# Performance work log

Measured on AMD Instinct MI355X. Metric: run time of the kernel, lower is better.

## Reference

```python
import jax, jax.numpy as jnp
import numpy as np

A = 5            # num_anchors
NC = 20          # num_classes
IGNORE_THRESH = 0.6
COORD_SCALE = 1.0
NOOBJ_SCALE = 1.0
OBJ_SCALE = 5.0
CLASS_SCALE = 1.0
ANCHORS_NP = np.array([[0.052, 0.066], [0.14, 0.11], [0.24, 0.30], [0.45, 0.42], [0.77, 0.72]], dtype=np.float32)


def setup_inputs() -> dict:
    key = jax.random.key(0)
    k1, k2, k3, k4, k5 = jax.random.split(key, 5)
    B, F, O = 32, 38, 50
    C = A * (5 + NC)
    outputs = jax.random.normal(k1, (B, C, F, F), jnp.float32)
    # targets: (cx, cy, w, h, cls) normalized; padded rows are all-zero
    cxy = jax.random.uniform(k2, (B, O, 2), minval=0.15, maxval=0.85)
    wh = jax.random.uniform(k3, (B, O, 2), minval=0.05, maxval=0.20)
    cls = jax.random.randint(k4, (B, O), 0, NC).astype(jnp.float32)
    targets = jnp.concatenate([cxy, wh, cls[..., None]], axis=-1)
    nobj = jax.random.randint(k5, (B,), 10, O + 1)
    valid = (jnp.arange(O)[None, :] < nobj[:, None]).astype(jnp.float32)
    targets = targets * valid[..., None]
    return {"outputs": outputs, "targets": targets, "anchors": jnp.asarray(ANCHORS_NP)}


def _pairwise_iou_xywh(a, b):
    # a: (..., N, 4), b: (..., M, 4) center-format -> IoU (..., N, M)
    a = a[..., :, None, :]
    b = b[..., None, :, :]
    tl = jnp.maximum(a[..., :2] - a[..., 2:] * 0.5, b[..., :2] - b[..., 2:] * 0.5)
    br = jnp.minimum(a[..., :2] + a[..., 2:] * 0.5, b[..., :2] + b[..., 2:] * 0.5)
    wh = jnp.clip(br - tl, 0.0)
    inter = wh[..., 0] * wh[..., 1]
    area_a = a[..., 2] * a[..., 3]
    area_b = b[..., 2] * b[..., 3]
    return inter / (area_a + area_b - inter + 1e-12)


def _forward(outputs, targets, anchors):
    B, C, F, _ = outputs.shape
    S = F * F
    O = targets.shape[1]
    valid = targets.sum(axis=2) > 0                    # (B, O)
    gt = targets[..., :4] * F                          # grid-unit cxywh
    gt_cls = targets[..., 4]

    out5 = outputs.reshape(B, A, 5 + NC, F, F)
    jj = jnp.arange(F, dtype=outputs.dtype)            # x (last axis)
    ii = jnp.arange(F, dtype=outputs.dtype)[:, None]   # y
    aw = (anchors[:, 0] * F)[None, :, None, None]
    ah = (anchors[:, 1] * F)[None, :, None, None]
    px = jax.nn.sigmoid(out5[:, :, 0]) + jj
    py = jax.nn.sigmoid(out5[:, :, 1]) + ii
    pw = jnp.exp(out5[:, :, 2]) * aw
    ph = jnp.exp(out5[:, :, 3]) * ah
    pred_boxes = jnp.stack([px, py, pw, ph], -1).transpose(0, 2, 3, 1, 4).reshape(B, S * A, 4)

    # anchor prior boxes at cell centers: (S, A, 4)
    ax = jnp.broadcast_to(jj + 0.5, (F, F))
    ay = jnp.broadcast_to(ii + 0.5, (F, F))
    aa = jnp.stack([
        jnp.broadcast_to(ax[:, :, None], (F, F, A)),
        jnp.broadcast_to(ay[:, :, None], (F, F, A)),
        jnp.broadcast_to((anchors[:, 0] * F)[None, None, :], (F, F, A)),
        jnp.broadcast_to((anchors[:, 1] * F)[None, None, :], (F, F, A)),
    ], -1).reshape(S, A, 4)

    ious = _pairwise_iou_xywh(pred_boxes, gt)          # (B, S*A, O)
    ious = jnp.where(valid[:, None, :], ious, 0.0)     # padded objs excluded (IoU >= 0)
    max_iou = ious.reshape(B, S, A, O).max(axis=-1)    # (B, S, A)

    n_pos = jnp.any(max_iou > IGNORE_THRESH, axis=(1, 2))
    iou_mask = jnp.full((B, S, A), NOOBJ_SCALE, outputs.dtype)
    iou_mask = jnp.where(n_pos[:, None, None] & (max_iou >= IGNORE_THRESH), 0.0, iou_mask)

    overlaps = _pairwise_iou_xywh(aa.reshape(1, S * A, 4), gt).reshape(B, S, A, O)

    # responsible cell: floor of top-left corner (faithful to source), anchor = argmax prior overlap
    x1y1 = gt[..., :2] - gt[..., 2:] * 0.5
    cxcy = jnp.floor(x1y1).astype(jnp.int32)
    cell = jnp.clip(cxcy[..., 1] * F + cxcy[..., 0], 0, S - 1)             # (B, O)
    ovT = overlaps.transpose(0, 3, 1, 2)                                   # (B, O, S, A)
    ov_cell = jnp.take_along_axis(ovT, cell[:, :, None, None], axis=2)[:, :, 0, :]
    anchor_idx = jnp.argmax(ov_cell, axis=-1)                              # (B, O)
    resp = aa[cell, anchor_idx]                                            # (B, O, 4)
    deltas = jnp.stack([gt[..., 0] - resp[..., 0], gt[..., 1] - resp[..., 1],
                        gt[..., 2] / resp[..., 2], gt[..., 3] / resp[..., 3]], -1)
    mi = jnp.take_along_axis(jnp.take_along_axis(max_iou, cell[:, :, None], axis=1),
                             anchor_idx[:, :, None], axis=2)[..., 0]       # (B, O)

    b_rep = jnp.broadcast_to(jnp.arange(B)[:, None], (B, O))
    cell_s = jnp.where(valid, cell, S)  # OOB index for padded objs -> dropped
    zt = jnp.zeros((B, S, A), outputs.dtype)
    box_target = jnp.zeros((B, S, A, 4), outputs.dtype).at[b_rep, cell_s, anchor_idx].set(deltas, mode='drop')
    box_mask = zt.at[b_rep, cell_s, anchor_idx].set(1.0, mode='drop')
    class_target = zt.at[b_rep, cell_s, anchor_idx].set(gt_cls, mode='drop')
    class_mask = zt.at[b_rep, cell_s, anchor_idx].set(1.0, mode='drop')
    iou_target = zt.at[b_rep, cell_s, anchor_idx].set(mi, mode='drop')
    iou_mask = iou_mask.at[b_rep, cell_s, anchor_idx].set(OBJ_SCALE, mode='drop')

    # prediction side, layout (B, (i*F+j)*A + a, 5+NC) matching target layout
    outs = out5.transpose(0, 3, 4, 1, 2).reshape(B, S * A, 5 + NC)
    pd = jnp.concatenate([jax.nn.sigmoid(outs[..., :2]), jnp.exp(outs[..., 2:4])], -1)
    conf = jax.nn.sigmoid(outs[..., 4])
    probs = jax.nn.softmax(outs[..., 5:], axis=-1)

    bm = box_mask.reshape(B, S * A, 1)
    im = iou_mask.reshape(B, S * A)
    box_loss = jnp.sum((pd * bm - box_target.reshape(B, S * A, 4) * bm) ** 2)
    iou_loss = jnp.sum((conf * im - iou_target.reshape(B, S * A) * im) ** 2)
    # faithful quirk of the source: cross-entropy applied to softmax *outputs* as logits
    ls = jax.nn.log_softmax(probs, axis=-1)
    ct = class_target.reshape(B, S * A).astype(jnp.int32)
    ce = -jnp.take_along_axis(ls, ct[..., None], axis=-1)[..., 0]
    class_loss = jnp.sum(ce * class_mask.reshape(B, S * A))
    return (COORD_SCALE * box_loss + iou_loss + CLASS_SCALE * class_loss) / B


def reference(outputs, targets, anchors):
    return _forward(outputs, targets, anchors)
```

## Files before the change

kernel.cpp:

```cpp
#include <hip/hip_runtime.h>
#include <math.h>

#define A_N 5
#define NC 20
#define FD 38
#define SD (FD*FD)
#define BD 32
#define OD 50
#define SA (SD*A_N)
#define GX ((SA + 255) / 256)
#define NBLK (BD * GX)
#define IGN_T 0.6f
#define OBJ_S 5.0f

__device__ __forceinline__ float sigm(float x) { return 1.0f / (1.0f + __expf(-x)); }

__global__ __launch_bounds__(256) void k_main(
    const float* __restrict__ outputs, const float* __restrict__ targets,
    const float* __restrict__ anchors,
    float* __restrict__ pbase, float* __restrict__ pcorr, int* __restrict__ pflag,
    float* __restrict__ out)
{
    __shared__ float  s_traw[OD * 5];
    __shared__ float4 g_box[OD];
    __shared__ float  g_den[OD];
    __shared__ float  s_anc[2 * A_N];
    __shared__ int    s_cnt, s_any;
    __shared__ float  wb[4], wc[4];

    const int b = blockIdx.y;
    const int tid = threadIdx.x;
    if (tid == 0) { s_cnt = 0; s_any = 0; }
    if (tid < OD * 5)  s_traw[tid] = targets[b * (OD * 5) + tid];
    if (tid < 2 * A_N) s_anc[tid]  = anchors[tid];
    if (blockIdx.x == 0 && b == 0 && tid == 0) *out = 0.0f;

    const int idx = blockIdx.x * 256 + tid;
    const bool act = (idx < SA);
    const int a = idx / SD, s = idx - a * SD;
    const int i = s / FD, j = s - i * FD;
    const float* ob = outputs + ((size_t)b * (A_N * 25) + a * 25) * SD + s;
    float q0 = 0, q1 = 0, q2 = 0, q3 = 0, q4 = 0;
    if (act) { q0 = ob[0]; q1 = ob[SD]; q2 = ob[2*SD]; q3 = ob[3*SD]; q4 = ob[4*SD]; }
    __syncthreads();

    if (tid < OD) {
        float tx = s_traw[tid*5], ty = s_traw[tid*5+1], tw = s_traw[tid*5+2];
        float th = s_traw[tid*5+3], tc = s_traw[tid*5+4];
        if (tx + ty + tw + th + tc > 0.0f) {
            float gx = tx * FD, gy = ty * FD, gw = tw * FD, gh = th * FD;
            int k = atomicAdd(&s_cnt, 1);
            g_box[k] = make_float4(gx - gw*0.5f, gy - gh*0.5f, gx + gw*0.5f, gy + gh*0.5f);
            g_den[k] = gw * gh + 1e-12f;
        }
    }
    __syncthreads();
    const int cnt = s_cnt;

    float base = 0.0f, corr = 0.0f;
    bool hot = false;
    if (act) {
        float aw = s_anc[2*a] * FD, ah = s_anc[2*a+1] * FD;
        float px = sigm(q0) + (float)j;
        float py = sigm(q1) + (float)i;
        float pw = __expf(q2) * aw;
        float ph = __expf(q3) * ah;
        float tlx = px - pw*0.5f, tly = py - ph*0.5f;
        float brx = px + pw*0.5f, bry = py + ph*0.5f;
        float ar = pw * ph;
        float bn = 0.0f, bd = 1.0f;
        for (int o = 0; o < cnt; ++o) {
            float4 bx = g_box[o];
            float w = fmaxf(fminf(brx, bx.z) - fmaxf(tlx, bx.x), 0.0f);
            float h = fmaxf(fminf(bry, bx.w) - fmaxf(tly, bx.y), 0.0f);
            float in = w * h, de = ar + g_den[o] - in;
            if (in * bd > bn * de) { bn = in; bd = de; }
        }
        float t = IGN_T * bd;
        hot = (bn > t);
        float conf = sigm(q4);
        float c2 = conf * conf;
        if (bn >= t) corr += c2;
        else         base += c2;
    }

    unsigned long long bal = __ballot(hot);
    if ((tid & 63) == 0 && bal) atomicOr(&s_any, 1);

    #pragma unroll
    for (int off = 32; off > 0; off >>= 1) {
        base += __shfl_down(base, off);
        corr += __shfl_down(corr, off);
    }
    int lane = tid & 63, w = tid >> 6;
    if (lane == 0) { wb[w] = base; wc[w] = corr; }
    __syncthreads();
    if (tid == 0) {
        int gid = b * GX + blockIdx.x;
        pbase[gid] = wb[0] + wb[1] + wb[2] + wb[3];
        pcorr[gid] = wc[0] + wc[1] + wc[2] + wc[3];
        pflag[gid] = s_any;
    }
}

__global__ __launch_bounds__(64) void k_rf(
    const float* __restrict__ outputs, const float* __restrict__ targets,
    const float* __restrict__ anchors,
    const float* __restrict__ pbase, const float* __restrict__ pcorr,
    const int* __restrict__ pflag, float* __restrict__ out)
{
    __shared__ float  s_traw[OD * 5];
    __shared__ float4 g_box[OD];
    __shared__ float  g_den[OD];
    __shared__ float  s_anc[2 * A_N];
    __shared__ int    s_key[OD];
    __shared__ int    s_cnt;

    const int b = blockIdx.x;
    const int lane = threadIdx.x;
    if (lane == 0) s_cnt = 0;
    for (int t = lane; t < OD * 5; t += 64) s_traw[t] = targets[b * (OD * 5) + t];
    if (lane < 2 * A_N) s_anc[lane] = anchors[lane];
    __syncthreads();

    float gx = 0, gy = 0, gw = 0, gh = 0;
    int ct = 0, key = -1;
    if (lane < OD) {
        float tx = s_traw[lane*5], ty = s_traw[lane*5+1], tw = s_traw[lane*5+2];
        float th = s_traw[lane*5+3], tc = s_traw[lane*5+4];
        if (tx + ty + tw + th + tc > 0.0f) {
            gx = tx * FD; gy = ty * FD; gw = tw * FD; gh = th * FD;
            float gtlx = gx - gw*0.5f, gtly = gy - gh*0.5f;
            float gbrx = gx + gw*0.5f, gbry = gy + gh*0.5f;
            int k = atomicAdd(&s_cnt, 1);
            g_box[k] = make_float4(gtlx, gtly, gbrx, gbry);
            g_den[k] = gw * gh + 1e-12f;
            int cx = (int)floorf(gtlx), cy = (int)floorf(gtly);
            int cell = min(max(cy * FD + cx, 0), SD - 1);
            int ci = cell / FD, cj = cell - ci * FD;
            float acx = (float)cj + 0.5f, acy = (float)ci + 0.5f;
            float areaB = gw * gh;
            float best = -1.0f; int bi = 0;
            for (int a = 0; a < A_N; ++a) {
                float aw = s_anc[2*a] * FD, ah = s_anc[2*a+1] * FD;
                float w = fmaxf(fminf(acx + aw*0.5f, gbrx) - fmaxf(acx - aw*0.5f, gtlx), 0.0f);
                float h = fmaxf(fminf(acy + ah*0.5f, gbry) - fmaxf(acy - ah*0.5f, gtly), 0.0f);
                float inter = w * h;
                float iou = inter / (aw*ah + areaB - inter + 1e-12f);
                if (iou > best) { best = iou; bi = a; }
            }
            key = bi * SD + cell;
            ct = (int)tc;
        }
    }
    if (lane < OD) s_key[lane] = key;
    __syncthreads();
    const int cnt = s_cnt;

    float rbase = 0.0f, rcorr = 0.0f;
    if (lane < OD && key >= 0) {
        int win = -1;
        #pragma unroll 10
        for (int o = 0; o < OD; ++o) win = (s_key[o] == key) ? o : win;
        if (win == lane) {
            int a = key / SD, cell = key - a * SD;
            int ci = cell / FD, cj = cell - ci * FD;
            const float* ob = outputs + ((size_t)b * (A_N * 25) + a * 25) * SD + cell;
            float o0 = ob[0], o1 = ob[SD], o2 = ob[2*SD], o3 = ob[3*SD], o4 = ob[4*SD];
            float aw = s_anc[2*a] * FD, ah = s_anc[2*a+1] * FD;
            float px = sigm(o0) + (float)cj;
            float py = sigm(o1) + (float)ci;
            float ew = __expf(o2), eh = __expf(o3);
            float pw = ew * aw, ph = eh * ah;
            float tlx = px - pw*0.5f, tly = py - ph*0.5f;
            float brx = px + pw*0.5f, bry = py + ph*0.5f;
            float ar = pw * ph;
            float bn = 0.0f, bd = 1.0f;
            for (int o = 0; o < cnt; ++o) {
                float4 bx = g_box[o];
                float w = fmaxf(fminf(brx, bx.z) - fmaxf(tlx, bx.x), 0.0f);
                float h = fmaxf(fminf(bry, bx.w) - fmaxf(tly, bx.y), 0.0f);
                float in = w * h, de = ar + g_den[o] - in;
                if (in * bd > bn * de) { bn = in; bd = de; }
            }
            float mi = bn / bd;
            float conf = sigm(o4);
            float d = conf - mi;
            rbase += OBJ_S * OBJ_S * d * d;
            float c2 = conf * conf;
            if (bn >= IGN_T * bd) rcorr -= c2;
            else                  rbase -= c2;
            float dx = gx - ((float)cj + 0.5f);
            float dy = gy - ((float)ci + 0.5f);
            float e0 = sigm(o0) - dx;
            float e1 = sigm(o1) - dy;
            float e2 = ew - gw / aw;
            float e3 = eh - gh / ah;
            rbase += e0*e0 + e1*e1 + e2*e2 + e3*e3;
            float x[NC];
            float xmax = -INFINITY;
            #pragma unroll
            for (int k = 0; k < NC; ++k) { x[k] = ob[(5 + k) * SD]; xmax = fmaxf(xmax, x[k]); }
            float esum = 0.0f;
            #pragma unroll
            for (int k = 0; k < NC; ++k) { x[k] = __expf(x[k] - xmax); esum += x[k]; }
            float inv = 1.0f / esum;
            float pmax = 0.0f, pct = 0.0f;
            #pragma unroll
            for (int k = 0; k < NC; ++k) {
                float p = x[k] * inv; x[k] = p;
                pmax = fmaxf(pmax, p);
                pct = (k == ct) ? p : pct;
            }
            float e2s = 0.0f;
            #pragma unroll
            for (int k = 0; k < NC; ++k) e2s += __expf(x[k] - pmax);
            rbase += -(pct - (pmax + __logf(e2s)));
        }
    }

    float pb = 0.0f, pc = 0.0f;
    int fl = 0;
    if (lane < GX) {
        pb = pbase[b * GX + lane];
        pc = pcorr[b * GX + lane];
        fl = pflag[b * GX + lane];
    }
    int np = (__ballot(fl != 0) != 0ull) ? 1 : 0;
    float sb = rbase + pb, sc = rcorr + pc;
    #pragma unroll
    for (int off = 32; off > 0; off >>= 1) {
        sb += __shfl_down(sb, off);
        sc += __shfl_down(sc, off);
    }
    if (lane == 0) {
        float total = sb + (np ? 0.0f : sc);
        atomicAdd(out, total * (1.0f / (float)BD));
    }
}

extern "C" void kernel_launch(void* const* d_in, const int* in_sizes, int n_in,
                              void* d_out, int out_size, void* d_ws, size_t ws_size,
                              hipStream_t stream) {
    (void)in_sizes; (void)n_in; (void)out_size; (void)ws_size;
    const float* outputs = (const float*)d_in[0];
    const float* targets = (const float*)d_in[1];
    const float* anchors = (const float*)d_in[2];
    float* out = (float*)d_out;

    float* pbase = (float*)d_ws;
    float* pcorr = pbase + NBLK;
    int*   pflag = (int*)(pcorr + NBLK);

    k_main<<<dim3(GX, BD), 256, 0, stream>>>(outputs, targets, anchors,
                                             pbase, pcorr, pflag, out);
    k_rf<<<dim3(BD), 64, 0, stream>>>(outputs, targets, anchors,
                                      pbase, pcorr, pflag, out);
}
```

Before: 83.84 us.

## Fold responsible-anchor work into main kernel and process two predictions per thread

The per-batch responsible-anchor computation moves from the second kernel into an extra block of the main grid, so it runs alongside the IoU scan. Each main-kernel thread now handles two anchor-cells, sharing every ground-truth box load across both IoU computations and halving the number of blocks. The second kernel becomes a tiny single-block reduction that writes the output directly, which removes the atomic add and the zero-initialisation. In exchange, parallelism per batch drops to 15 blocks plus one serial-ish block per batch, and the extra block adds latency to the critical path.

```diff
diff --git a/kernel.cpp b/kernel.cpp
--- a/kernel.cpp
+++ b/kernel.cpp
@@ -8,8 +8,10 @@
 #define BD 32
 #define OD 50
 #define SA (SD*A_N)
-#define GX ((SA + 255) / 256)
-#define NBLK (BD * GX)
+#define HALF (SA/2)
+#define GXP 15
+#define SLOTB 16
+#define NSLOT (BD * SLOTB)
 #define IGN_T 0.6f
 #define OBJ_S 5.0f
 
@@ -18,35 +20,152 @@
 __global__ __launch_bounds__(256) void k_main(
     const float* __restrict__ outputs, const float* __restrict__ targets,
     const float* __restrict__ anchors,
-    float* __restrict__ pbase, float* __restrict__ pcorr, int* __restrict__ pflag,
-    float* __restrict__ out)
+    float* __restrict__ pbase, float* __restrict__ pcorr, int* __restrict__ pflag)
 {
-    __shared__ float  s_traw[OD * 5];
     __shared__ float4 g_box[OD];
     __shared__ float  g_den[OD];
     __shared__ float  s_anc[2 * A_N];
     __shared__ int    s_cnt, s_any;
+    __shared__ int    s_key[OD];
     __shared__ float  wb[4], wc[4];
 
     const int b = blockIdx.y;
     const int tid = threadIdx.x;
     if (tid == 0) { s_cnt = 0; s_any = 0; }
-    if (tid < OD * 5)  s_traw[tid] = targets[b * (OD * 5) + tid];
-    if (tid < 2 * A_N) s_anc[tid]  = anchors[tid];
-    if (blockIdx.x == 0 && b == 0 && tid == 0) *out = 0.0f;
-
-    const int idx = blockIdx.x * 256 + tid;
-    const bool act = (idx < SA);
-    const int a = idx / SD, s = idx - a * SD;
-    const int i = s / FD, j = s - i * FD;
-    const float* ob = outputs + ((size_t)b * (A_N * 25) + a * 25) * SD + s;
-    float q0 = 0, q1 = 0, q2 = 0, q3 = 0, q4 = 0;
-    if (act) { q0 = ob[0]; q1 = ob[SD]; q2 = ob[2*SD]; q3 = ob[3*SD]; q4 = ob[4*SD]; }
-    __syncthreads();
-
+    if (tid < 2 * A_N) s_anc[tid] = anchors[tid];
+
+    if (blockIdx.x == GXP) {
+        __syncthreads();
+        float gx = 0, gy = 0, gw = 0, gh = 0;
+        int ct = 0, key = -1;
+        if (tid < OD) {
+            const float* t = targets + (b * OD + tid) * 5;
+            float tx = t[0], ty = t[1], tw = t[2], th = t[3], tc = t[4];
+            if (tx + ty + tw + th + tc > 0.0f) {
+                gx = tx * FD; gy = ty * FD; gw = tw * FD; gh = th * FD;
+                float gtlx = gx - gw*0.5f, gtly = gy - gh*0.5f;
+                float gbrx = gx + gw*0.5f, gbry = gy + gh*0.5f;
+                int k = atomicAdd(&s_cnt, 1);
+                g_box[k] = make_float4(gtlx, gtly, gbrx, gbry);
+                g_den[k] = gw * gh + 1e-12f;
+                int cx = (int)floorf(gtlx), cy = (int)floorf(gtly);
+                int cell = min(max(cy * FD + cx, 0), SD - 1);
+                int ci = cell / FD, cj = cell - ci * FD;
+                float acx = (float)cj + 0.5f, acy = (float)ci + 0.5f;
+                float areaB = gw * gh;
+                float best = -1.0f; int bi = 0;
+                for (int a = 0; a < A_N; ++a) {
+                    float aw = s_anc[2*a] * FD, ah = s_anc[2*a+1] * FD;
+                    float w = fmaxf(fminf(acx + aw*0.5f, gbrx) - fmaxf(acx - aw*0.5f, gtlx), 0.0f);
+                    float h = fmaxf(fminf(acy + ah*0.5f, gbry) - fmaxf(acy - ah*0.5f, gtly), 0.0f);
+                    float inter = w * h;
+                    float iou = inter / (aw*ah + areaB - inter + 1e-12f);
+                    if (iou > best) { best = iou; bi = a; }
+                }
+                key = bi * SD + cell;
+                ct = (int)tc;
+            }
+        }
+        if (tid < OD) s_key[tid] = key;
+        __syncthreads();
+        const int cnt = s_cnt;
+
+        float rbase = 0.0f, rcorr = 0.0f;
+        if (tid < OD && key >= 0) {
+            int win = -1;
+            #pragma unroll 10
+            for (int o = 0; o < OD; ++o) win = (s_key[o] == key) ? o : win;
+            if (win == tid) {
+                int a = key / SD, cell = key - a * SD;
+                int ci = cell / FD, cj = cell - ci * FD;
+                const float* ob = outputs + ((size_t)b * (A_N * 25) + a * 25) * SD + cell;
+                float o0 = ob[0], o1 = ob[SD], o2 = ob[2*SD], o3 = ob[3*SD], o4 = ob[4*SD];
+                float aw = s_anc[2*a] * FD, ah = s_anc[2*a+1] * FD;
+                float px = sigm(o0) + (float)cj;
+                float py = sigm(o1) + (float)ci;
+                float ew = __expf(o2), eh = __expf(o3);
+                float pw = ew * aw, ph = eh * ah;
+                float tlx = px - pw*0.5f, tly = py - ph*0.5f;
+                float brx = px + pw*0.5f, bry = py + ph*0.5f;
+                float ar = pw * ph;
+                float bn = 0.0f, bd = 1.0f;
+                for (int o = 0; o < cnt; ++o) {
+                    float4 bx = g_box[o];
+                    float w = fmaxf(fminf(brx, bx.z) - fmaxf(tlx, bx.x), 0.0f);
+                    float h = fmaxf(fminf(bry, bx.w) - fmaxf(tly, bx.y), 0.0f);
+                    float in = w * h, de = ar + g_den[o] - in;
+                    if (in * bd > bn * de) { bn = in; bd = de; }
+                }
+                float mi = bn / bd;
+                float conf = sigm(o4);
+                float d = conf - mi;
+                rbase += OBJ_S * OBJ_S * d * d;
+                float c2 = conf * conf;
+                if (bn >= IGN_T * bd) rcorr -= c2;
+                else                  rbase -= c2;
+                float dx = gx - ((float)cj + 0.5f);
+                float dy = gy - ((float)ci + 0.5f);
+                float e0 = sigm(o0) - dx;
+                float e1 = sigm(o1) - dy;
+                float e2 = ew - gw / aw;
+                float e3 = eh - gh / ah;
+                rbase += e0*e0 + e1*e1 + e2*e2 + e3*e3;
+                float x[NC];
+                float xmax = -INFINITY;
+                #pragma unroll
+                for (int k = 0; k < NC; ++k) { x[k] = ob[(5 + k) * SD]; xmax = fmaxf(xmax, x[k]); }
+                float esum = 0.0f;
+                #pragma unroll
+                for (int k = 0; k < NC; ++k) { x[k] = __expf(x[k] - xmax); esum += x[k]; }
+                float inv = 1.0f / esum;
+                float pmax = 0.0f, pct = 0.0f;
+                #pragma unroll
+                for (int k = 0; k < NC; ++k) {
+                    float p = x[k] * inv; x[k] = p;
+                    pmax = fmaxf(pmax, p);
+                    pct = (k == ct) ? p : pct;
+                }
+                float e2s = 0.0f;
+                #pragma unroll
+                for (int k = 0; k < NC; ++k) e2s += __expf(x[k] - pmax);
+                rbase += -(pct - (pmax + __logf(e2s)));
+            }
+        }
+        #pragma unroll
+        for (int off = 32; off > 0; off >>= 1) {
+            rbase += __shfl_down(rbase, off);
+            rcorr += __shfl_down(rcorr, off);
+        }
+        int lane = tid & 63, w = tid >> 6;
+        if (lane == 0) { wb[w] = rbase; wc[w] = rcorr; }
+        __syncthreads();
+        if (tid == 0) {
+            int gid = b * SLOTB + GXP;
+            pbase[gid] = wb[0] + wb[1] + wb[2] + wb[3];
+            pcorr[gid] = wc[0] + wc[1] + wc[2] + wc[3];
+            pflag[gid] = 0;
+        }
+        return;
+    }
+
+    const int ix = blockIdx.x * 256 + tid;
+    const bool act = (ix < HALF);
+    const int p0 = ix, p1 = ix + HALF;
+    int a0 = p0 / SD, r0 = p0 - a0 * SD;
+    int a1 = p1 / SD, r1 = p1 - a1 * SD;
+    int ii0 = r0 / FD, jj0 = r0 - ii0 * FD;
+    int ii1 = r1 / FD, jj1 = r1 - ii1 * FD;
+    const float* ob0 = outputs + ((size_t)b * (A_N * 25) + a0 * 25) * SD + r0;
+    const float* ob1 = outputs + ((size_t)b * (A_N * 25) + a1 * 25) * SD + r1;
+    float q00 = 0, q01 = 0, q02 = 0, q03 = 0, q04 = 0;
+    float q10 = 0, q11 = 0, q12 = 0, q13 = 0, q14 = 0;
+    if (act) {
+        q00 = ob0[0]; q01 = ob0[SD]; q02 = ob0[2*SD]; q03 = ob0[3*SD]; q04 = ob0[4*SD];
+        q10 = ob1[0]; q11 = ob1[SD]; q12 = ob1[2*SD]; q13 = ob1[3*SD]; q14 = ob1[4*SD];
+    }
     if (tid < OD) {
-        float tx = s_traw[tid*5], ty = s_traw[tid*5+1], tw = s_traw[tid*5+2];
-        float th = s_traw[tid*5+3], tc = s_traw[tid*5+4];
+        const float* t = targets + (b * OD + tid) * 5;
+        float tx = t[0], ty = t[1], tw = t[2], th = t[3], tc = t[4];
         if (tx + ty + tw + th + tc > 0.0f) {
             float gx = tx * FD, gy = ty * FD, gw = tw * FD, gh = th * FD;
             int k = atomicAdd(&s_cnt, 1);
@@ -60,28 +179,37 @@
     float base = 0.0f, corr = 0.0f;
     bool hot = false;
     if (act) {
-        float aw = s_anc[2*a] * FD, ah = s_anc[2*a+1] * FD;
-        float px = sigm(q0) + (float)j;
-        float py = sigm(q1) + (float)i;
-        float pw = __expf(q2) * aw;
-        float ph = __expf(q3) * ah;
-        float tlx = px - pw*0.5f, tly = py - ph*0.5f;
-        float brx = px + pw*0.5f, bry = py + ph*0.5f;
-        float ar = pw * ph;
-        float bn = 0.0f, bd = 1.0f;
+        float aw0 = s_anc[2*a0] * FD, ah0 = s_anc[2*a0+1] * FD;
+        float aw1 = s_anc[2*a1] * FD, ah1 = s_anc[2*a1+1] * FD;
+        float px0 = sigm(q00) + (float)jj0, py0 = sigm(q01) + (float)ii0;
+        float px1 = sigm(q10) + (float)jj1, py1 = sigm(q11) + (float)ii1;
+        float pw0 = __expf(q02) * aw0, ph0 = __expf(q03) * ah0;
+        float pw1 = __expf(q12) * aw1, ph1 = __expf(q13) * ah1;
+        float tlx0 = px0 - pw0*0.5f, tly0 = py0 - ph0*0.5f;
+        float brx0 = px0 + pw0*0.5f, bry0 = py0 + ph0*0.5f;
+        float tlx1 = px1 - pw1*0.5f, tly1 = py1 - ph1*0.5f;
+        float brx1 = px1 + pw1*0.5f, bry1 = py1 + ph1*0.5f;
+        float ar0 = pw0 * ph0, ar1 = pw1 * ph1;
+
+        float bn0 = 0.0f, bd0 = 1.0f, bn1 = 0.0f, bd1 = 1.0f;
         for (int o = 0; o < cnt; ++o) {
             float4 bx = g_box[o];
-            float w = fmaxf(fminf(brx, bx.z) - fmaxf(tlx, bx.x), 0.0f);
-            float h = fmaxf(fminf(bry, bx.w) - fmaxf(tly, bx.y), 0.0f);
-            float in = w * h, de = ar + g_den[o] - in;
-            if (in * bd > bn * de) { bn = in; bd = de; }
-        }
-        float t = IGN_T * bd;
-        hot = (bn > t);
-        float conf = sigm(q4);
-        float c2 = conf * conf;
-        if (bn >= t) corr += c2;
-        else         base += c2;
+            float dn = g_den[o];
+            float w0 = fmaxf(fminf(brx0, bx.z) - fmaxf(tlx0, bx.x), 0.0f);
+            float h0 = fmaxf(fminf(bry0, bx.w) - fmaxf(tly0, bx.y), 0.0f);
+            float in0 = w0 * h0, de0 = ar0 + dn - in0;
+            if (in0 * bd0 > bn0 * de0) { bn0 = in0; bd0 = de0; }
+            float w1 = fmaxf(fminf(brx1, bx.z) - fmaxf(tlx1, bx.x), 0.0f);
+            float h1 = fmaxf(fminf(bry1, bx.w) - fmaxf(tly1, bx.y), 0.0f);
+            float in1 = w1 * h1, de1 = ar1 + dn - in1;
+            if (in1 * bd1 > bn1 * de1) { bn1 = in1; bd1 = de1; }
+        }
+        float t0 = IGN_T * bd0, t1 = IGN_T * bd1;
+        hot = (bn0 > t0) || (bn1 > t1);
+        float c0 = sigm(q04); c0 *= c0;
+        float c1 = sigm(q14); c1 *= c1;
+        if (bn0 >= t0) corr += c0; else base += c0;
+        if (bn1 >= t1) corr += c1; else base += c1;
     }
 
     unsigned long long bal = __ballot(hot);
@@ -96,147 +224,35 @@
     if (lane == 0) { wb[w] = base; wc[w] = corr; }
     __syncthreads();
     if (tid == 0) {
-        int gid = b * GX + blockIdx.x;
+        int gid = b * SLOTB + blockIdx.x;
         pbase[gid] = wb[0] + wb[1] + wb[2] + wb[3];
         pcorr[gid] = wc[0] + wc[1] + wc[2] + wc[3];
         pflag[gid] = s_any;
     }
 }
 
-__global__ __launch_bounds__(64) void k_rf(
-    const float* __restrict__ outputs, const float* __restrict__ targets,
-    const float* __restrict__ anchors,
+__global__ __launch_bounds__(256) void k_fin(
     const float* __restrict__ pbase, const float* __restrict__ pcorr,
     const int* __restrict__ pflag, float* __restrict__ out)
 {
-    __shared__ float  s_traw[OD * 5];
-    __shared__ float4 g_box[OD];
-    __shared__ float  g_den[OD];
-    __shared__ float  s_anc[2 * A_N];
-    __shared__ int    s_key[OD];
-    __shared__ int    s_cnt;
-
-    const int b = blockIdx.x;
-    const int lane = threadIdx.x;
-    if (lane == 0) s_cnt = 0;
-    for (int t = lane; t < OD * 5; t += 64) s_traw[t] = targets[b * (OD * 5) + t];
-    if (lane < 2 * A_N) s_anc[lane] = anchors[lane];
-    __syncthreads();
-
-    float gx = 0, gy = 0, gw = 0, gh = 0;
-    int ct = 0, key = -1;
-    if (lane < OD) {
-        float tx = s_traw[lane*5], ty = s_traw[lane*5+1], tw = s_traw[lane*5+2];
-        float th = s_traw[lane*5+3], tc = s_traw[lane*5+4];
-        if (tx + ty + tw + th + tc > 0.0f) {
-            gx = tx * FD; gy = ty * FD; gw = tw * FD; gh = th * FD;
-            float gtlx = gx - gw*0.5f, gtly = gy - gh*0.5f;
-            float gbrx = gx + gw*0.5f, gbry = gy + gh*0.5f;
-            int k = atomicAdd(&s_cnt, 1);
-            g_box[k] = make_float4(gtlx, gtly, gbrx, gbry);
-            g_den[k] = gw * gh + 1e-12f;
-            int cx = (int)floorf(gtlx), cy = (int)floorf(gtly);
-            int cell = min(max(cy * FD + cx, 0), SD - 1);
-            int ci = cell / FD, cj = cell - ci * FD;
-            float acx = (float)cj + 0.5f, acy = (float)ci + 0.5f;
-            float areaB = gw * gh;
-            float best = -1.0f; int bi = 0;
-            for (int a = 0; a < A_N; ++a) {
-                float aw = s_anc[2*a] * FD, ah = s_anc[2*a+1] * FD;
-                float w = fmaxf(fminf(acx + aw*0.5f, gbrx) - fmaxf(acx - aw*0.5f, gtlx), 0.0f);
-                float h = fmaxf(fminf(acy + ah*0.5f, gbry) - fmaxf(acy - ah*0.5f, gtly), 0.0f);
-                float inter = w * h;
-                float iou = inter / (aw*ah + areaB - inter + 1e-12f);
-                if (iou > best) { best = iou; bi = a; }
-            }
-            key = bi * SD + cell;
-            ct = (int)tc;
-        }
-    }
-    if (lane < OD) s_key[lane] = key;
-    __syncthreads();
-    const int cnt = s_cnt;
-
-    float rbase = 0.0f, rcorr = 0.0f;
-    if (lane < OD && key >= 0) {
-        int win = -1;
-        #pragma unroll 10
-        for (int o = 0; o < OD; ++o) win = (s_key[o] == key) ? o : win;
-        if (win == lane) {
-            int a = key / SD, cell = key - a * SD;
-            int ci = cell / FD, cj = cell - ci * FD;
-            const float* ob = outputs + ((size_t)b * (A_N * 25) + a * 25) * SD + cell;
-            float o0 = ob[0], o1 = ob[SD], o2 = ob[2*SD], o3 = ob[3*SD], o4 = ob[4*SD];
-            float aw = s_anc[2*a] * FD, ah = s_anc[2*a+1] * FD;
-            float px = sigm(o0) + (float)cj;
-            float py = sigm(o1) + (float)ci;
-            float ew = __expf(o2), eh = __expf(o3);
-            float pw = ew * aw, ph = eh * ah;
-            float tlx = px - pw*0.5f, tly = py - ph*0.5f;
-            float brx = px + pw*0.5f, bry = py + ph*0.5f;
-            float ar = pw * ph;
-            float bn = 0.0f, bd = 1.0f;
-            for (int o = 0; o < cnt; ++o) {
-                float4 bx = g_box[o];
-                float w = fmaxf(fminf(brx, bx.z) - fmaxf(tlx, bx.x), 0.0f);
-                float h = fmaxf(fminf(bry, bx.w) - fmaxf(tly, bx.y), 0.0f);
-                float in = w * h, de = ar + g_den[o] - in;
-                if (in * bd > bn * de) { bn = in; bd = de; }
-            }
-            float mi = bn / bd;
-            float conf = sigm(o4);
-            float d = conf - mi;
-            rbase += OBJ_S * OBJ_S * d * d;
-            float c2 = conf * conf;
-            if (bn >= IGN_T * bd) rcorr -= c2;
-            else                  rbase -= c2;
-            float dx = gx - ((float)cj + 0.5f);
-            float dy = gy - ((float)ci + 0.5f);
-            float e0 = sigm(o0) - dx;
-            float e1 = sigm(o1) - dy;
-            float e2 = ew - gw / aw;
-            float e3 = eh - gh / ah;
-            rbase += e0*e0 + e1*e1 + e2*e2 + e3*e3;
-            float x[NC];
-            float xmax = -INFINITY;
-            #pragma unroll
-            for (int k = 0; k < NC; ++k) { x[k] = ob[(5 + k) * SD]; xmax = fmaxf(xmax, x[k]); }
-            float esum = 0.0f;
-            #pragma unroll
-            for (int k = 0; k < NC; ++k) { x[k] = __expf(x[k] - xmax); esum += x[k]; }
-            float inv = 1.0f / esum;
-            float pmax = 0.0f, pct = 0.0f;
-            #pragma unroll
-            for (int k = 0; k < NC; ++k) {
-                float p = x[k] * inv; x[k] = p;
-                pmax = fmaxf(pmax, p);
-                pct = (k == ct) ? p : pct;
-            }
-            float e2s = 0.0f;
-            #pragma unroll
-            for (int k = 0; k < NC; ++k) e2s += __expf(x[k] - pmax);
-            rbase += -(pct - (pmax + __logf(e2s)));
-        }
-    }
-
-    float pb = 0.0f, pc = 0.0f;
-    int fl = 0;
-    if (lane < GX) {
-        pb = pbase[b * GX + lane];
-        pc = pcorr[b * GX + lane];
-        fl = pflag[b * GX + lane];
-    }
-    int np = (__ballot(fl != 0) != 0ull) ? 1 : 0;
-    float sb = rbase + pb, sc = rcorr + pc;
+    __shared__ int npos[BD];
+    __shared__ float wsum[4];
+    const int tid = threadIdx.x;
+    if (tid < BD) {
+        int f = 0;
+        for (int x = 0; x < SLOTB; ++x) f |= pflag[tid * SLOTB + x];
+        npos[tid] = f;
+    }
+    __syncthreads();
+    float s = 0.0f;
+    for (int g = tid; g < NSLOT; g += 256)
+        s += pbase[g] + (npos[g >> 4] ? 0.0f : pcorr[g]);
     #pragma unroll
-    for (int off = 32; off > 0; off >>= 1) {
-        sb += __shfl_down(sb, off);
-        sc += __shfl_down(sc, off);
-    }
-    if (lane == 0) {
-        float total = sb + (np ? 0.0f : sc);
-        atomicAdd(out, total * (1.0f / (float)BD));
-    }
+    for (int off = 32; off > 0; off >>= 1) s += __shfl_down(s, off);
+    int lane = tid & 63, w = tid >> 6;
+    if (lane == 0) wsum[w] = s;
+    __syncthreads();
+    if (tid == 0) out[0] = (wsum[0] + wsum[1] + wsum[2] + wsum[3]) * (1.0f / (float)BD);
 }
 
 extern "C" void kernel_launch(void* const* d_in, const int* in_sizes, int n_in,
@@ -249,11 +265,10 @@
     float* out = (float*)d_out;
 
     float* pbase = (float*)d_ws;
-    float* pcorr = pbase + NBLK;
-    int*   pflag = (int*)(pcorr + NBLK);
-
-    k_main<<<dim3(GX, BD), 256, 0, stream>>>(outputs, targets, anchors,
-                                             pbase, pcorr, pflag, out);
-    k_rf<<<dim3(BD), 64, 0, stream>>>(outputs, targets, anchors,
-                                      pbase, pcorr, pflag, out);
+    float* pcorr = pbase + NSLOT;
+    int*   pflag = (int*)(pcorr + NSLOT);
+
+    k_main<<<dim3(GXP + 1, BD), 256, 0, stream>>>(outputs, targets, anchors,
+                                                  pbase, pcorr, pflag);
+    k_fin<<<dim3(1), 256, 0, stream>>>(pbase, pcorr, pflag, out);
 }
```

After: 76.68 us. -8.5%, faster.
